# Kernel optimization log

Measured on AMD Instinct MI355X. Metric: run time of the kernel, lower is better.

The kernel has to match this reference:

```python
import jax, jax.numpy as jnp
import numpy as np

NUM_TOKENS = 8192
DIM = 256
BETA = 0.25
DECAY = 0.99
EPS = 1e-05


def setup_inputs() -> dict:
    key = jax.random.key(0)
    k1, k2 = jax.random.split(key, 2)
    z = jax.random.normal(k1, (16, DIM, 32, 32), dtype=jnp.float32)
    embedding = jax.random.normal(k2, (NUM_TOKENS, DIM), dtype=jnp.float32)
    cluster_size = jnp.zeros((NUM_TOKENS,), dtype=jnp.float32)
    ema_w = embedding  # module init copies embed_init into both embedding and ema_w
    return {"z": z, "embedding": embedding, "cluster_size": cluster_size, "ema_w": ema_w}


def reference(z, embedding, cluster_size, ema_w):
    # z: [B, D, H, W] -> [B, H, W, D]
    zp = jnp.transpose(z, (0, 2, 3, 1))
    zf = zp.reshape(-1, DIM)  # [N, D]
    # squared euclidean distances [N, K] via ||z||^2 + ||e||^2 - 2 z.e
    d = (jnp.sum(zf * zf, axis=1, keepdims=True)
         + jnp.sum(embedding * embedding, axis=1)
         - 2.0 * (zf @ embedding.T))
    idx = jnp.argmin(d, axis=1)  # [N]
    z_q = embedding[idx].reshape(zp.shape)  # [B, H, W, D]

    # training-mode EMA statistics (pure-functional: returned as new states)
    counts = jax.ops.segment_sum(jnp.ones(zf.shape[0], dtype=zf.dtype), idx,
                                 num_segments=NUM_TOKENS)
    embed_sum = jax.ops.segment_sum(zf, idx, num_segments=NUM_TOKENS)  # [K, D]
    cs = cluster_size * DECAY + (1.0 - DECAY) * counts
    new_ema_w = ema_w * DECAY + (1.0 - DECAY) * embed_sum
    # torch evaluates sum AFTER add_(eps): denom = sum(cs + eps) + K*eps
    cs = cs + EPS
    new_cluster_size = cs / (jnp.sum(cs) + NUM_TOKENS * EPS)
    new_embedding = new_ema_w / new_cluster_size[:, None]

    loss = BETA * jnp.mean((jax.lax.stop_gradient(z_q) - zp) ** 2)
    # straight-through estimator
    z_q_st = zp + jax.lax.stop_gradient(z_q - zp)
    out = jnp.transpose(z_q_st, (0, 3, 1, 2))  # back to [B, D, H, W]
    return out, loss, idx, new_cluster_size, new_ema_w, new_embedding
```

## Files before the change

### kernel.cpp

```cpp
#include <hip/hip_runtime.h>

#define N_TOK   16384
#define K_CODES 8192
#define DIMS    256

#define OUT_OFF  0
#define LOSS_OFF 4194304
#define IDX_OFF  4194305
#define NCS_OFF  4210689
#define NEMA_OFF 4218881
#define NEMB_OFF 6316033

#define WS_ZFRAG  0u
#define WS_EFRAG  16777216u
#define WS_ENORM  25165824u
#define WS_PVAL   25198592u
#define WS_PIDX   25460736u
#define WS_IDXI   25722880u
#define WS_CNT    25788416u
#define WS_CS     25821184u
#define WS_OFFS   25853952u
#define WS_WPOS   25886720u
#define WS_TLIST  25919488u
#define WS_DENOM  25985024u

typedef _Float16 f16x8 __attribute__((ext_vector_type(8)));
typedef float    f32x16 __attribute__((ext_vector_type(16)));

union HU { _Float16 h; unsigned short u; };

static __device__ inline void split_f32(float x, unsigned short& hi, unsigned short& lo) {
    HU a; a.h = (_Float16)x;
    float r = (x - (float)a.h) * 2048.0f;
    HU b; b.h = (_Float16)r;
    hi = a.u; lo = b.u;
}

static __device__ inline float join_f16(unsigned short h, unsigned short l) {
    HU a, b; a.u = h; b.u = l;
    return (float)a.h + (float)b.h * 4.8828125e-4f;
}

#define GLD16(gp, lp) __builtin_amdgcn_global_load_lds( \
    (const __attribute__((address_space(1))) unsigned int*)(gp), \
    (__attribute__((address_space(3))) unsigned int*)(lp), 16, 0, 0)

__global__ __launch_bounds__(256) void cvt_z_kernel(const float* __restrict__ z,
                                                    unsigned short* __restrict__ zfrag,
                                                    float* __restrict__ loss_cell,
                                                    double* __restrict__ denom) {
    __shared__ float T[64][65];
    const int t = threadIdx.x;
    const int hg = blockIdx.x & 15, dg = (blockIdx.x >> 4) & 3, b = blockIdx.x >> 6;
    if (blockIdx.x == 0 && t == 0) { *loss_cell = 0.f; *denom = 0.0; }
    const int c4 = (t & 15) * 4, r0 = t >> 4;
    const float* zb = z + (((size_t)(b * 256 + dg * 64)) << 10) + hg * 64;
#pragma unroll
    for (int p = 0; p < 4; ++p) {
        const int r = r0 + p * 16;
        const float4 v = *(const float4*)(zb + ((size_t)r << 10) + c4);
        T[r][c4] = v.x; T[r][c4 + 1] = v.y; T[r][c4 + 2] = v.z; T[r][c4 + 3] = v.w;
    }
    __syncthreads();
    const int tr = t & 63, dc = (t >> 6) * 16;
    const int tile = b * 16 + hg;
    const int tg = tile * 2 + (tr >> 5), l31 = tr & 31;
    const int ks = dg * 4 + (dc >> 4);
    unsigned short hb[16], lb[16];
#pragma unroll
    for (int j = 0; j < 16; ++j) split_f32(T[dc + j][tr], hb[j], lb[j]);
#pragma unroll
    for (int lv = 0; lv < 2; ++lv) {
        const unsigned short* src = lv ? lb : hb;
        unsigned short* dst = zfrag + (size_t)((tg * 2 + lv) * 16 + ks) * 512;
        *(uint4*)(dst + l31 * 8)       = ((const uint4*)src)[0];
        *(uint4*)(dst + 256 + l31 * 8) = ((const uint4*)src)[1];
    }
}

__global__ __launch_bounds__(256) void cvt_e_enorm(const float* __restrict__ emb,
                                                   unsigned short* __restrict__ efrag,
                                                   float* __restrict__ enorm,
                                                   int* __restrict__ cnt) {
    __shared__ double red[256];
    const int t = threadIdx.x, g = blockIdx.x;
    const int lane = t & 63, q = t >> 6;
    const int l31 = lane & 31, lhi = lane >> 5;
    if (g < 32) cnt[g * 256 + t] = 0;
    const float* rowp = emb + (size_t)(g * 32 + l31) * 256 + lhi * 8;
    double s = 0.0;
#pragma unroll
    for (int kk = 0; kk < 4; ++kk) {
        const int ks = q * 4 + kk;
        const float4 a = *(const float4*)(rowp + ks * 16);
        const float4 bq = *(const float4*)(rowp + ks * 16 + 4);
        const float vv[8] = {a.x, a.y, a.z, a.w, bq.x, bq.y, bq.z, bq.w};
        unsigned short hb[8], lb[8];
#pragma unroll
        for (int j = 0; j < 8; ++j) {
            split_f32(vv[j], hb[j], lb[j]);
            s += (double)vv[j] * (double)vv[j];
        }
        *(uint4*)(efrag + (size_t)((g * 2 + 0) * 16 + ks) * 512 + lane * 8) = *(const uint4*)hb;
        *(uint4*)(efrag + (size_t)((g * 2 + 1) * 16 + ks) * 512 + lane * 8) = *(const uint4*)lb;
    }
    red[t] = s;
    __syncthreads();
    if (t < 32) {
        double acc = 0.0;
#pragma unroll
        for (int qq = 0; qq < 4; ++qq) acc += red[qq * 64 + t] + red[qq * 64 + 32 + t];
        enorm[g * 32 + t] = (float)acc;
    }
}

__global__ __launch_bounds__(256, 2) void argmin_mfma(
    const unsigned short* __restrict__ zfrag, const unsigned short* __restrict__ efrag,
    const float* __restrict__ enorm, float* __restrict__ pval, int* __restrict__ pidx) {
    __shared__ __align__(16) unsigned short E[4][8192];
    __shared__ __align__(16) float en_all[2048];

    const int tid = threadIdx.x, lane = tid & 63, wave = tid >> 6;
    const int tile = blockIdx.x & 127, csplit = blockIdx.x >> 7;
    const int token0 = tile * 128, code0 = csplit * 2048;

    f16x8 Zr[2][16];
    {
        const unsigned short* zb = zfrag + (size_t)(tile * 4 + wave) * 16384 + lane * 8;
#pragma unroll
        for (int lv = 0; lv < 2; ++lv)
#pragma unroll
            for (int ks = 0; ks < 16; ++ks)
                Zr[lv][ks] = *(const f16x8*)(zb + (lv * 16 + ks) * 512);
    }

    const int slv = wave >> 1, scg = wave & 1;

    auto stage = [&](int ch) {
        const int g = csplit * 64 + (ch >> 2) * 2 + scg;
        const int nkc = ch & 3;
#pragma unroll
        for (int ksl = 0; ksl < 4; ++ksl) {
            const unsigned short* sp = efrag +
                (size_t)((g * 2 + slv) * 16 + nkc * 4 + ksl) * 512 + lane * 8;
            GLD16(sp, &E[ch & 3][(wave * 4 + ksl) * 512]);
        }
    };

#pragma unroll
    for (int c = 0; c < 2; ++c) {
        const float* sp = enorm + code0 + (wave * 2 + c) * 256 + lane * 4;
        GLD16(sp, &en_all[(wave * 2 + c) * 256]);
    }
    stage(0);
    stage(1);

    float bv = 3.4e38f; int bi = 0;

    for (int ct = 0; ct < 32; ++ct) {
        f32x16 acc_h[2], acc_l[2];
#pragma unroll
        for (int cg = 0; cg < 2; ++cg)
#pragma unroll
            for (int qq = 0; qq < 16; ++qq) { acc_h[cg][qq] = 0.f; acc_l[cg][qq] = 0.f; }

#pragma unroll
        for (int kc = 0; kc < 4; ++kc) {
            if (kc <= 1) {
                stage(ct * 4 + kc + 2);
                asm volatile("s_waitcnt vmcnt(8)" ::: "memory");
            } else if (ct < 31) {
                stage(ct * 4 + kc + 2);
                asm volatile("s_waitcnt vmcnt(8)" ::: "memory");
            } else if (kc == 2) {
                asm volatile("s_waitcnt vmcnt(4)" ::: "memory");
            } else {
                asm volatile("s_waitcnt vmcnt(0)" ::: "memory");
            }
            __builtin_amdgcn_s_barrier();
            __builtin_amdgcn_sched_barrier(0);

            __builtin_amdgcn_s_setprio(1);
#pragma unroll
            for (int ksl = 0; ksl < 4; ++ksl) {
                const int ks = kc * 4 + ksl;
                f16x8 ae[2][2];
#pragma unroll
                for (int lv = 0; lv < 2; ++lv)
#pragma unroll
                    for (int cg = 0; cg < 2; ++cg)
                        ae[lv][cg] = *(const f16x8*)&E[kc][((lv * 2 + cg) * 4 + ksl) * 512 + lane * 8];
#pragma unroll
                for (int cg = 0; cg < 2; ++cg) {
                    acc_h[cg] = __builtin_amdgcn_mfma_f32_32x32x16_f16(ae[0][cg], Zr[0][ks], acc_h[cg], 0, 0, 0);
                    acc_l[cg] = __builtin_amdgcn_mfma_f32_32x32x16_f16(ae[0][cg], Zr[1][ks], acc_l[cg], 0, 0, 0);
                    acc_l[cg] = __builtin_amdgcn_mfma_f32_32x32x16_f16(ae[1][cg], Zr[0][ks], acc_l[cg], 0, 0, 0);
                }
            }
            __builtin_amdgcn_s_setprio(0);

            if (kc == 3) {
                const int rbase = 4 * (lane >> 5);
#pragma unroll
                for (int cg = 0; cg < 2; ++cg)
#pragma unroll
                    for (int r = 0; r < 16; ++r) {
                        const int cl = cg * 32 + (r & 3) + 8 * (r >> 2) + rbase;
                        const float s = en_all[ct * 64 + cl] -
                            2.0f * (acc_h[cg][r] + acc_l[cg][r] * 4.8828125e-4f);
                        const int code = code0 + ct * 64 + cl;
                        if (s < bv) { bv = s; bi = code; }
                    }
            }
        }
    }
    {
        const float ov = __shfl_xor(bv, 32);
        const int   oi = __shfl_xor(bi, 32);
        if (ov < bv || (ov == bv && oi < bi)) { bv = ov; bi = oi; }
    }
    if (lane < 32) {
        const int n = token0 + wave * 32 + lane;
        pval[csplit * N_TOK + n] = bv;
        pidx[csplit * N_TOK + n] = bi;
    }
}

__global__ __launch_bounds__(256) void combine4_kernel(
    const float* __restrict__ pval, const int* __restrict__ pidx,
    int* __restrict__ idx_i, float* __restrict__ idx_f, int* __restrict__ cnt) {
    const int n = blockIdx.x * 256 + threadIdx.x;
    float bv = pval[n]; int bi = pidx[n];
#pragma unroll
    for (int s = 1; s < 4; ++s) {
        const float v = pval[s * N_TOK + n];
        const int i = pidx[s * N_TOK + n];
        if (v < bv || (v == bv && i < bi)) { bv = v; bi = i; }
    }
    idx_i[n] = bi;
    idx_f[n] = (float)bi;
    atomicAdd(&cnt[bi], 1);
}

__global__ __launch_bounds__(256) void scan_kernel(const int* __restrict__ cnt,
                                                   int* __restrict__ offs,
                                                   int* __restrict__ wpos) {
    __shared__ int part[256];
    const int tid = threadIdx.x;
    const int base = tid * 32;
    int loc[32];
    int s = 0;
#pragma unroll
    for (int j = 0; j < 32; ++j) { loc[j] = cnt[base + j]; s += loc[j]; }
    part[tid] = s;
    __syncthreads();
    for (int off = 1; off < 256; off <<= 1) {
        int v = 0;
        if (tid >= off) v = part[tid - off];
        __syncthreads();
        if (tid >= off) part[tid] += v;
        __syncthreads();
    }
    int run = (tid > 0) ? part[tid - 1] : 0;
#pragma unroll
    for (int j = 0; j < 32; ++j) {
        offs[base + j] = run;
        wpos[base + j] = run;
        run += loc[j];
    }
}

__global__ __launch_bounds__(256) void scatter_cs(
    const int* __restrict__ idx_i, int* __restrict__ wpos, int* __restrict__ tlist,
    const float* __restrict__ cluster_size, const int* __restrict__ cnt,
    float* __restrict__ cs, double* __restrict__ denom) {
    __shared__ double red[256];
    const int t = threadIdx.x, b = blockIdx.x;
    if (b < 64) {
        const int n = b * 256 + t;
        const int k = idx_i[n];
        tlist[atomicAdd(&wpos[k], 1)] = n;
    } else {
        const int k = (b - 64) * 256 + t;
        const float v = cluster_size[k] * 0.99f + 0.01f * (float)cnt[k] + 1e-5f;
        cs[k] = v;
        red[t] = (double)v;
        __syncthreads();
        for (int s2 = 128; s2; s2 >>= 1) {
            if (t < s2) red[t] += red[t + s2];
            __syncthreads();
        }
        if (t == 0) atomicAdd(denom, red[0]);
    }
}

__global__ __launch_bounds__(256) void nema_gather(
    const unsigned short* __restrict__ zfrag,
    const int* __restrict__ offs, const int* __restrict__ cnt, const int* __restrict__ tlist,
    const float* __restrict__ ema_w, const float* __restrict__ cs,
    const double* __restrict__ denom, float* __restrict__ ncs_out,
    float* __restrict__ nema_out, float* __restrict__ nemb_out,
    const float* __restrict__ z, const float* __restrict__ emb,
    const int* __restrict__ idx_i, float* __restrict__ out, float* __restrict__ loss_cell) {
    __shared__ float redf[256];
    const int t = threadIdx.x;
    if (blockIdx.x < 2048) {
        const int lane = t & 63, wave = t >> 6;
        const int k = blockIdx.x * 4 + wave;
        const int l31 = lane & 31, sel = lane >> 5;
        const int beg = offs[k], c = cnt[k];
        float acc[8] = {0.f, 0.f, 0.f, 0.f, 0.f, 0.f, 0.f, 0.f};
        for (int i = 0; i < c; ++i) {
            const int tok = tlist[beg + i];
            const int tg = tok >> 5, tl = tok & 31;
            const uint4 v = *(const uint4*)(zfrag +
                (size_t)((tg * 2 + sel) * 16 + (l31 >> 1)) * 512 + (l31 & 1) * 256 + tl * 8);
            uint4 o;
            o.x = __shfl_xor((int)v.x, 32); o.y = __shfl_xor((int)v.y, 32);
            o.z = __shfl_xor((int)v.z, 32); o.w = __shfl_xor((int)v.w, 32);
            if (lane < 32) {
                const unsigned short* hp = (const unsigned short*)&v;
                const unsigned short* lp = (const unsigned short*)&o;
#pragma unroll
                for (int j = 0; j < 8; ++j) acc[j] += join_f16(hp[j], lp[j]);
            }
        }
        const float dn = (float)(*denom) + (float)K_CODES * 1e-5f;
        const float ncs = cs[k] / dn;
        if (lane == 0) ncs_out[k] = ncs;
        if (lane < 32) {
            const size_t off = ((size_t)k << 8) + l31 * 8;
#pragma unroll
            for (int j = 0; j < 8; ++j) {
                const float ne = ema_w[off + j] * 0.99f + 0.01f * acc[j];
                nema_out[off + j] = ne;
                nemb_out[off + j] = ne / ncs;
            }
        }
    } else {
        const int gb = blockIdx.x - 2048;
        const int n0 = (gb >> 2) * 64;
        const int dg = (gb & 3) * 64;
        const int b = n0 >> 10, hw0 = n0 & 1023;
        const int lane = t & 63, w = t >> 6;
        const int n = n0 + lane;
        const int k = idx_i[n];
        const float* zb = z + ((size_t)b << 18) + hw0 + lane;
        float* ob = out + ((size_t)b << 18) + hw0 + lane;
        float ls = 0.f;
#pragma unroll 4
        for (int d = dg + w; d < dg + 64; d += 4) {
            const float zv = zb[(size_t)d << 10];
            const float ev = emb[((size_t)k << 8) + d];
            ob[(size_t)d << 10] = ev;
            const float df = ev - zv;
            ls += df * df;
        }
        redf[t] = ls;
        __syncthreads();
        for (int s2 = 128; s2; s2 >>= 1) {
            if (t < s2) redf[t] += redf[t + s2];
            __syncthreads();
        }
        if (t == 0) atomicAdd(loss_cell, redf[0] * (0.25f / 4194304.0f));
    }
}

extern "C" void kernel_launch(void* const* d_in, const int* in_sizes, int n_in,
                              void* d_out, int out_size, void* d_ws, size_t ws_size,
                              hipStream_t stream) {
    const float* z            = (const float*)d_in[0];
    const float* emb          = (const float*)d_in[1];
    const float* cluster_size = (const float*)d_in[2];
    const float* ema_w        = (const float*)d_in[3];
    float* out = (float*)d_out;
    char*  wsb = (char*)d_ws;

    unsigned short* zfrag = (unsigned short*)(wsb + WS_ZFRAG);
    unsigned short* efrag = (unsigned short*)(wsb + WS_EFRAG);
    float*  enorm  = (float*)(wsb + WS_ENORM);
    float*  pval   = (float*)(wsb + WS_PVAL);
    int*    pidx   = (int*)(wsb + WS_PIDX);
    int*    idx_i  = (int*)(wsb + WS_IDXI);
    int*    cnt    = (int*)(wsb + WS_CNT);
    float*  cs     = (float*)(wsb + WS_CS);
    int*    offs   = (int*)(wsb + WS_OFFS);
    int*    wpos   = (int*)(wsb + WS_WPOS);
    int*    tlist  = (int*)(wsb + WS_TLIST);
    double* denom  = (double*)(wsb + WS_DENOM);

    cvt_z_kernel<<<1024, 256, 0, stream>>>(z, zfrag, out + LOSS_OFF, denom);
    cvt_e_enorm<<<256, 256, 0, stream>>>(emb, efrag, enorm, cnt);
    argmin_mfma<<<512, 256, 0, stream>>>(zfrag, efrag, enorm, pval, pidx);
    combine4_kernel<<<N_TOK / 256, 256, 0, stream>>>(pval, pidx, idx_i,
                                                     out + IDX_OFF, cnt);
    scan_kernel<<<1, 256, 0, stream>>>(cnt, offs, wpos);
    scatter_cs<<<96, 256, 0, stream>>>(idx_i, wpos, tlist, cluster_size, cnt, cs, denom);
    nema_gather<<<3072, 256, 0, stream>>>(zfrag, offs, cnt, tlist, ema_w, cs, denom,
                                          out + NCS_OFF, out + NEMA_OFF, out + NEMB_OFF,
                                          z, emb, idx_i, out + OUT_OFF, out + LOSS_OFF);
}
```

Baseline: 425.9 us.

## Deepen LDS prefetch and double-buffer fragment reads in MFMA argmin loop

Restructures the argmin MFMA main loop so global-to-LDS staging runs three chunks ahead instead of two. LDS fragment reads are ping-ponged between two register sets so each read overlaps the previous MFMA group, and the barrier moves to the end of each chunk. Block IDs are also remapped so that neighbouring blocks spread across code splits. The aim is to hide LDS and global load latency behind MFMA work, at the cost of more registers and a riskier 4-slot buffer reuse.

```diff
diff --git a/kernel.cpp b/kernel.cpp
--- a/kernel.cpp
+++ b/kernel.cpp
@@ -121,7 +121,8 @@
     __shared__ __align__(16) float en_all[2048];
 
     const int tid = threadIdx.x, lane = tid & 63, wave = tid >> 6;
-    const int tile = blockIdx.x & 127, csplit = blockIdx.x >> 7;
+    const int bid = ((blockIdx.x & 7) << 6) | (blockIdx.x >> 3);
+    const int tile = bid & 127, csplit = bid >> 7;
     const int token0 = tile * 128, code0 = csplit * 2048;
 
     f16x8 Zr[2][16];
@@ -152,13 +153,28 @@
         const float* sp = enorm + code0 + (wave * 2 + c) * 256 + lane * 4;
         GLD16(sp, &en_all[(wave * 2 + c) * 256]);
     }
-    stage(0);
-    stage(1);
+    stage(0); stage(1); stage(2);
+    asm volatile("s_waitcnt vmcnt(4)" ::: "memory");
+    __builtin_amdgcn_s_barrier();
 
     float bv = 3.4e38f; int bi = 0;
+    f32x16 acc_h[2], acc_l[2];
+    f16x8 aeP[4], aeQ[4];
+
+    auto mm = [&](const f16x8* ae, int ks) {
+#pragma unroll
+        for (int cg = 0; cg < 2; ++cg) {
+            acc_h[cg] = __builtin_amdgcn_mfma_f32_32x32x16_f16(ae[cg],     Zr[0][ks], acc_h[cg], 0, 0, 0);
+            acc_l[cg] = __builtin_amdgcn_mfma_f32_32x32x16_f16(ae[cg],     Zr[1][ks], acc_l[cg], 0, 0, 0);
+            acc_l[cg] = __builtin_amdgcn_mfma_f32_32x32x16_f16(ae[2 + cg], Zr[0][ks], acc_l[cg], 0, 0, 0);
+        }
+    };
+
+#pragma unroll
+    for (int f = 0; f < 4; ++f)
+        aeP[f] = *(const f16x8*)&E[0][(f * 4 + 0) * 512 + lane * 8];
 
     for (int ct = 0; ct < 32; ++ct) {
-        f32x16 acc_h[2], acc_l[2];
 #pragma unroll
         for (int cg = 0; cg < 2; ++cg)
 #pragma unroll
@@ -166,38 +182,27 @@
 
 #pragma unroll
         for (int kc = 0; kc < 4; ++kc) {
-            if (kc <= 1) {
-                stage(ct * 4 + kc + 2);
-                asm volatile("s_waitcnt vmcnt(8)" ::: "memory");
-            } else if (ct < 31) {
-                stage(ct * 4 + kc + 2);
-                asm volatile("s_waitcnt vmcnt(8)" ::: "memory");
-            } else if (kc == 2) {
-                asm volatile("s_waitcnt vmcnt(4)" ::: "memory");
-            } else {
-                asm volatile("s_waitcnt vmcnt(0)" ::: "memory");
+            if (ct < 31 || kc == 0) stage(ct * 4 + kc + 3);
+
+#pragma unroll
+            for (int f = 0; f < 4; ++f)
+                aeQ[f] = *(const f16x8*)&E[kc][(f * 4 + 1) * 512 + lane * 8];
+            mm(aeP, kc * 4 + 0);
+#pragma unroll
+            for (int f = 0; f < 4; ++f)
+                aeP[f] = *(const f16x8*)&E[kc][(f * 4 + 2) * 512 + lane * 8];
+            mm(aeQ, kc * 4 + 1);
+#pragma unroll
+            for (int f = 0; f < 4; ++f)
+                aeQ[f] = *(const f16x8*)&E[kc][(f * 4 + 3) * 512 + lane * 8];
+            mm(aeP, kc * 4 + 2);
+            {
+                const int nb = (kc + 1) & 3;
+#pragma unroll
+                for (int f = 0; f < 4; ++f)
+                    aeP[f] = *(const f16x8*)&E[nb][(f * 4 + 0) * 512 + lane * 8];
             }
-            __builtin_amdgcn_s_barrier();
-            __builtin_amdgcn_sched_barrier(0);
-
-            __builtin_amdgcn_s_setprio(1);
-#pragma unroll
-            for (int ksl = 0; ksl < 4; ++ksl) {
-                const int ks = kc * 4 + ksl;
-                f16x8 ae[2][2];
-#pragma unroll
-                for (int lv = 0; lv < 2; ++lv)
-#pragma unroll
-                    for (int cg = 0; cg < 2; ++cg)
-                        ae[lv][cg] = *(const f16x8*)&E[kc][((lv * 2 + cg) * 4 + ksl) * 512 + lane * 8];
-#pragma unroll
-                for (int cg = 0; cg < 2; ++cg) {
-                    acc_h[cg] = __builtin_amdgcn_mfma_f32_32x32x16_f16(ae[0][cg], Zr[0][ks], acc_h[cg], 0, 0, 0);
-                    acc_l[cg] = __builtin_amdgcn_mfma_f32_32x32x16_f16(ae[0][cg], Zr[1][ks], acc_l[cg], 0, 0, 0);
-                    acc_l[cg] = __builtin_amdgcn_mfma_f32_32x32x16_f16(ae[1][cg], Zr[0][ks], acc_l[cg], 0, 0, 0);
-                }
-            }
-            __builtin_amdgcn_s_setprio(0);
+            mm(aeQ, kc * 4 + 3);
 
             if (kc == 3) {
                 const int rbase = 4 * (lane >> 5);
@@ -212,6 +217,11 @@
                         if (s < bv) { bv = s; bi = code; }
                     }
             }
+
+            __builtin_amdgcn_sched_barrier(0);
+            if (ct == 31 && kc != 0) asm volatile("s_waitcnt vmcnt(0)" ::: "memory");
+            else                     asm volatile("s_waitcnt vmcnt(4)" ::: "memory");
+            __builtin_amdgcn_s_barrier();
         }
     }
     {
```

After: 424.0 us. No clear change (-0.4%).

## Stream codebook fragments directly from global into registers, dropping LDS staging

Applied to the files above, without the earlier changes.

The argmin kernel no longer stages codebook fragments through a 4-deep LDS ring with barriers and vmcnt waits. Each wave now loads its codebook MFMA operands straight from global (L2) into a double-buffered register array, prefetching the next k-step while the current one computes. Blocks are remapped so that the four code splits of one token tile are adjacent in launch order, and the norm reads in the argmin epilogue are vectorized as float4. This removes the LDS traffic and block-wide barriers, but every wave now fetches the same codebook data separately, so L2 bandwidth and load latency become the limit, and register pressure rises.

```diff
diff --git a/kernel.cpp b/kernel.cpp
--- a/kernel.cpp
+++ b/kernel.cpp
@@ -117,11 +117,11 @@
 __global__ __launch_bounds__(256, 2) void argmin_mfma(
     const unsigned short* __restrict__ zfrag, const unsigned short* __restrict__ efrag,
     const float* __restrict__ enorm, float* __restrict__ pval, int* __restrict__ pidx) {
-    __shared__ __align__(16) unsigned short E[4][8192];
     __shared__ __align__(16) float en_all[2048];
 
     const int tid = threadIdx.x, lane = tid & 63, wave = tid >> 6;
-    const int tile = blockIdx.x & 127, csplit = blockIdx.x >> 7;
+    const int csplit = blockIdx.x & 3;
+    const int tile   = blockIdx.x >> 2;
     const int token0 = tile * 128, code0 = csplit * 2048;
 
     f16x8 Zr[2][16];
@@ -134,86 +134,72 @@
                 Zr[lv][ks] = *(const f16x8*)(zb + (lv * 16 + ks) * 512);
     }
 
-    const int slv = wave >> 1, scg = wave & 1;
-
-    auto stage = [&](int ch) {
-        const int g = csplit * 64 + (ch >> 2) * 2 + scg;
-        const int nkc = ch & 3;
-#pragma unroll
-        for (int ksl = 0; ksl < 4; ++ksl) {
-            const unsigned short* sp = efrag +
-                (size_t)((g * 2 + slv) * 16 + nkc * 4 + ksl) * 512 + lane * 8;
-            GLD16(sp, &E[ch & 3][(wave * 4 + ksl) * 512]);
-        }
-    };
-
 #pragma unroll
     for (int c = 0; c < 2; ++c) {
         const float* sp = enorm + code0 + (wave * 2 + c) * 256 + lane * 4;
         GLD16(sp, &en_all[(wave * 2 + c) * 256]);
     }
-    stage(0);
-    stage(1);
+    __syncthreads();
+
+    const char* ebase = (const char*)efrag + ((size_t)csplit << 21) + (size_t)(lane * 16);
+
+    f16x8 ae[2][4];
+    auto issue = [&](int c, f16x8* buf) {
+        const char* p = ebase + ((c >> 4) << 16) + ((c & 15) << 10);
+        buf[0] = *(const f16x8*)(p);
+        buf[1] = *(const f16x8*)(p + 32768);
+        buf[2] = *(const f16x8*)(p + 16384);
+        buf[3] = *(const f16x8*)(p + 49152);
+    };
 
     float bv = 3.4e38f; int bi = 0;
+    f32x16 acc_h[2], acc_l[2];
+
+    issue(0, ae[0]);
 
     for (int ct = 0; ct < 32; ++ct) {
-        f32x16 acc_h[2], acc_l[2];
 #pragma unroll
         for (int cg = 0; cg < 2; ++cg)
 #pragma unroll
             for (int qq = 0; qq < 16; ++qq) { acc_h[cg][qq] = 0.f; acc_l[cg][qq] = 0.f; }
 
 #pragma unroll
-        for (int kc = 0; kc < 4; ++kc) {
-            if (kc <= 1) {
-                stage(ct * 4 + kc + 2);
-                asm volatile("s_waitcnt vmcnt(8)" ::: "memory");
+        for (int j = 0; j < 16; ++j) {
+            if (j < 15) {
+                issue(ct * 16 + j + 1, ae[(j + 1) & 1]);
             } else if (ct < 31) {
-                stage(ct * 4 + kc + 2);
-                asm volatile("s_waitcnt vmcnt(8)" ::: "memory");
-            } else if (kc == 2) {
-                asm volatile("s_waitcnt vmcnt(4)" ::: "memory");
-            } else {
-                asm volatile("s_waitcnt vmcnt(0)" ::: "memory");
+                issue((ct + 1) * 16, ae[0]);
             }
-            __builtin_amdgcn_s_barrier();
-            __builtin_amdgcn_sched_barrier(0);
-
-            __builtin_amdgcn_s_setprio(1);
-#pragma unroll
-            for (int ksl = 0; ksl < 4; ++ksl) {
-                const int ks = kc * 4 + ksl;
-                f16x8 ae[2][2];
-#pragma unroll
-                for (int lv = 0; lv < 2; ++lv)
-#pragma unroll
-                    for (int cg = 0; cg < 2; ++cg)
-                        ae[lv][cg] = *(const f16x8*)&E[kc][((lv * 2 + cg) * 4 + ksl) * 512 + lane * 8];
-#pragma unroll
-                for (int cg = 0; cg < 2; ++cg) {
-                    acc_h[cg] = __builtin_amdgcn_mfma_f32_32x32x16_f16(ae[0][cg], Zr[0][ks], acc_h[cg], 0, 0, 0);
-                    acc_l[cg] = __builtin_amdgcn_mfma_f32_32x32x16_f16(ae[0][cg], Zr[1][ks], acc_l[cg], 0, 0, 0);
-                    acc_l[cg] = __builtin_amdgcn_mfma_f32_32x32x16_f16(ae[1][cg], Zr[0][ks], acc_l[cg], 0, 0, 0);
-                }
+            const f16x8* a = ae[j & 1];
+#pragma unroll
+            for (int cg = 0; cg < 2; ++cg) {
+                acc_h[cg] = __builtin_amdgcn_mfma_f32_32x32x16_f16(a[cg],     Zr[0][j], acc_h[cg], 0, 0, 0);
+                acc_l[cg] = __builtin_amdgcn_mfma_f32_32x32x16_f16(a[cg],     Zr[1][j], acc_l[cg], 0, 0, 0);
+                acc_l[cg] = __builtin_amdgcn_mfma_f32_32x32x16_f16(a[2 + cg], Zr[0][j], acc_l[cg], 0, 0, 0);
             }
-            __builtin_amdgcn_s_setprio(0);
-
-            if (kc == 3) {
-                const int rbase = 4 * (lane >> 5);
-#pragma unroll
-                for (int cg = 0; cg < 2; ++cg)
-#pragma unroll
-                    for (int r = 0; r < 16; ++r) {
-                        const int cl = cg * 32 + (r & 3) + 8 * (r >> 2) + rbase;
-                        const float s = en_all[ct * 64 + cl] -
+        }
+
+        {
+            const int rbase = 4 * (lane >> 5);
+#pragma unroll
+            for (int cg = 0; cg < 2; ++cg)
+#pragma unroll
+                for (int rq = 0; rq < 4; ++rq) {
+                    const int clb = cg * 32 + 8 * rq + rbase;
+                    const float4 en4 = *(const float4*)&en_all[ct * 64 + clb];
+                    const float* e4 = (const float*)&en4;
+#pragma unroll
+                    for (int jj = 0; jj < 4; ++jj) {
+                        const int r = rq * 4 + jj;
+                        const float s = e4[jj] -
                             2.0f * (acc_h[cg][r] + acc_l[cg][r] * 4.8828125e-4f);
-                        const int code = code0 + ct * 64 + cl;
+                        const int code = code0 + ct * 64 + clb + jj;
                         if (s < bv) { bv = s; bi = code; }
                     }
-            }
-        }
-    }
+                }
+        }
+    }
+
     {
         const float ov = __shfl_xor(bv, 32);
         const int   oi = __shfl_xor(bi, 32);
```

Measured after the change: 462.4 us. +8.6%, slower.
